# Kernel optimization log

Measured on AMD Instinct MI355X. Metric: run time of the kernel, lower is better.

## Reference

```python
import jax, jax.numpy as jnp
import numpy as np
import math

B, T, D = 2, 2048, 1024
H, HD = 16, 64          # num_heads, head_dim = D // H
ROPE, BASE = 64, 10000.0  # rope covers full head dim
GLOBAL_IDS = jnp.array([2, 3, 4, 5, 6, 7], dtype=jnp.int32)


def setup_inputs() -> dict:
    key = jax.random.key(0)
    k1, k2, k3, k4 = jax.random.split(key, 4)
    x = jax.random.normal(k1, (B, T, D), dtype=jnp.float32)
    input_ids = jax.random.randint(k2, (B, T), 0, 1024, dtype=jnp.int32)
    W_qkv = jax.random.normal(k3, (3 * H * HD, D), dtype=jnp.float32) * 0.02
    b_qkv = jnp.zeros((3 * H * HD,), dtype=jnp.float32)
    W_out = jax.random.normal(k4, (D, H * HD), dtype=jnp.float32) * 0.02
    b_out = jnp.zeros((D,), dtype=jnp.float32)
    return {"x": x, "input_ids": input_ids, "W_qkv": W_qkv, "b_qkv": b_qkv,
            "W_out": W_out, "b_out": b_out}


def _apply_rotary(x, cos, sin):
    # x: [B,H,T,HD]; rope covers first ROPE dims (= full head here)
    x_rot, x_pass = x[..., :ROPE], x[..., ROPE:]
    half = ROPE // 2
    x1, x2 = x_rot[..., :half], x_rot[..., half:]
    x1n = x1 * cos - x2 * sin
    x2n = x1 * sin + x2 * cos
    return jnp.concatenate([x1n, x2n, x_pass], axis=-1)


def reference(x, input_ids, W_qkv, b_qkv, W_out, b_out):
    Bx, Tx, _ = x.shape
    qkv = x @ W_qkv.T + b_qkv                      # [B,T,3*H*HD]
    q, k, v = jnp.split(qkv, 3, axis=-1)
    def heads(t):
        return t.reshape(Bx, Tx, H, HD).transpose(0, 2, 1, 3)  # [B,H,T,HD]
    q, k, v = heads(q), heads(k), heads(v)

    # RoPE
    pos = jnp.arange(Tx, dtype=jnp.float32)
    inv_freq = 1.0 / (BASE ** (jnp.arange(0, ROPE, 2, dtype=jnp.float32) / ROPE))
    freqs = pos[:, None] * inv_freq[None, :]        # [T, ROPE//2]
    cos, sin = jnp.cos(freqs)[None, None], jnp.sin(freqs)[None, None]
    q = _apply_rotary(q, cos, sin)
    k = _apply_rotary(k, cos, sin)

    # causal mask OR global-query rows (BigBird-style)
    causal = jnp.tril(jnp.ones((Tx, Tx), dtype=bool))[None, None]   # [1,1,T,T]
    global_mask = jnp.isin(input_ids, GLOBAL_IDS)                    # [B,T]
    allow = causal | global_mask[:, None, :, None]                   # [B,1,T,T]

    scale = math.sqrt(HD)
    logits = jnp.einsum('bhqd,bhkd->bhqk', q, k) / scale
    neg = -jnp.finfo(logits.dtype).max
    logits = jnp.where(allow, logits, neg)
    attn = jax.nn.softmax(logits, axis=-1)
    out = jnp.einsum('bhqk,bhkd->bhqd', attn, v)
    out = out.transpose(0, 2, 1, 3).reshape(Bx, Tx, H * HD)
    return out @ W_out.T + b_out
```

## Files before the change

### kernel.cpp

```cpp
#include <hip/hip_runtime.h>
#include <math.h>

#define Bc 2
#define Tc 2048
#define Dc 1024
#define Hc 16
#define HDc 64

typedef __attribute__((ext_vector_type(8))) short bf16x8;
typedef __attribute__((ext_vector_type(4))) float f32x4;
typedef __attribute__((ext_vector_type(16))) float f32x16;

__device__ __forceinline__ unsigned short f2bf(float f) {
    union { float f; unsigned int u; } v; v.f = f;
    unsigned int r = (v.u + 0x7FFFu + ((v.u >> 16) & 1u)) >> 16;
    return (unsigned short)r;
}
__device__ __forceinline__ unsigned pack2bf(float a, float b) {
    unsigned au = __float_as_uint(a) + 0x8000u;
    unsigned bu = __float_as_uint(b) + 0x8000u;
    return __builtin_amdgcn_perm(bu, au, 0x07060302u);
}

__device__ __forceinline__ void gload_lds16(const unsigned short* g,
                                            unsigned short* l) {
    __builtin_amdgcn_global_load_lds(
        (const __attribute__((address_space(1))) unsigned int*)g,
        (__attribute__((address_space(3))) unsigned int*)l,
        16, 0, 0);
}

#define CEXP 0.1803368801111204f

__global__ __launch_bounds__(256) void convert_bf16(
    const float* __restrict__ x, const float* __restrict__ wqkv,
    const float* __restrict__ wout,
    unsigned short* __restrict__ xb, unsigned short* __restrict__ wqkvb,
    unsigned short* __restrict__ woutb, float2* __restrict__ ropeTab)
{
    const int gid = blockIdx.x * 256 + threadIdx.x;
    if (gid < Tc * 32) {
        const int t = gid >> 5, i = gid & 31;
        const float freq = exp2f((float)i * -0.4152410118609203f);
        const float ang = (float)t * freq;
        ropeTab[gid] = make_float2(cosf(ang), sinf(ang));
    }
    const int i = gid * 4;
    const float* src; unsigned short* dst; int off;
    if (i < 4194304)      { src = x;    dst = xb;    off = i; }
    else if (i < 7340032) { src = wqkv; dst = wqkvb; off = i - 4194304; }
    else                  { src = wout; dst = woutb; off = i - 7340032; }
    float4 v = *(const float4*)&src[off];
    ushort4 o;
    o.x = f2bf(v.x); o.y = f2bf(v.y); o.z = f2bf(v.z); o.w = f2bf(v.w);
    *(ushort4*)&dst[off] = o;
}

template <int MODE>
__global__ __launch_bounds__(256) void gemm_mfma(
    const unsigned short* __restrict__ A, const unsigned short* __restrict__ W,
    const float* __restrict__ bias, float* __restrict__ C,
    unsigned short* __restrict__ Qp, unsigned short* __restrict__ Kp,
    unsigned short* __restrict__ Vtp, const float2* __restrict__ ropeTab,
    int M, int N, int K)
{
    __shared__ unsigned short Apk[128 * 8 * 8];
    __shared__ unsigned short Bpk[128 * 8 * 8];

    const int tid = threadIdx.x;
    const int lane = tid & 63;
    const int wave = tid >> 6;
    const int quad = lane >> 4;
    const int c = lane & 15;
    const int wm = wave >> 1;
    const int wn = wave & 1;
    const int m0 = blockIdx.y * 128;
    const int n0 = blockIdx.x * 128;

    f32x4 acc[4][4];
#pragma unroll
    for (int mt = 0; mt < 4; mt++)
#pragma unroll
        for (int nt = 0; nt < 4; nt++) acc[mt][nt] = (f32x4){0.f, 0.f, 0.f, 0.f};

    const int lrow = lane >> 3;
    const int srcoct = (lane & 7) ^ lrow;

    for (int k0 = 0; k0 < K; k0 += 64) {
        __syncthreads();
#pragma unroll
        for (int i = 0; i < 4; i++) {
            const int r = wave * 32 + i * 8 + lrow;
            gload_lds16(&A[(size_t)(m0 + r) * K + k0 + srcoct * 8],
                        &Apk[(wave * 32 + i * 8) * 64]);
            gload_lds16(&W[(size_t)(n0 + r) * K + k0 + srcoct * 8],
                        &Bpk[(wave * 32 + i * 8) * 64]);
        }
        __syncthreads();
#pragma unroll
        for (int ko = 0; ko < 2; ko++) {
            bf16x8 af[4], bf[4];
#pragma unroll
            for (int mt = 0; mt < 4; mt++) {
                const int m = wm * 64 + mt * 16 + c;
                af[mt] = *(const bf16x8*)&Apk[(m * 8 + ((ko * 4 + quad) ^ (m & 7))) * 8];
            }
#pragma unroll
            for (int nt = 0; nt < 4; nt++) {
                const int n = wn * 64 + nt * 16 + c;
                bf[nt] = *(const bf16x8*)&Bpk[(n * 8 + ((ko * 4 + quad) ^ (n & 7))) * 8];
            }
#pragma unroll
            for (int mt = 0; mt < 4; mt++)
#pragma unroll
                for (int nt = 0; nt < 4; nt++)
                    acc[mt][nt] = __builtin_amdgcn_mfma_f32_16x16x32_bf16(
                        af[mt], bf[nt], acc[mt][nt], 0, 0, 0);
        }
    }

    if (MODE == 0) {
#pragma unroll
        for (int mt = 0; mt < 4; mt++) {
            const int m = m0 + wm * 64 + mt * 16 + quad * 4;
#pragma unroll
            for (int nt = 0; nt < 4; nt++) {
                const int n = n0 + wn * 64 + nt * 16 + c;
                const float bv = bias[n];
#pragma unroll
                for (int reg = 0; reg < 4; reg++)
                    C[(size_t)(m + reg) * N + n] = acc[mt][nt][reg] + bv;
            }
        }
    } else {
        const int n_wave = n0 + wn * 64;
        const int which = n_wave >> 10;
        const int h = (n_wave >> 6) & 15;
        const int b = m0 >> 11;
        const int t_base = (m0 & 2047) + wm * 64;

        __syncthreads();
        unsigned short* stg = ((wave < 2) ? Apk : Bpk) + (wave & 1) * 4096;

        if (which < 2) {
            unsigned short* dst = (which == 0) ? Qp : Kp;
#pragma unroll
            for (int mt = 0; mt < 4; mt++) {
#pragma unroll
                for (int nt = 0; nt < 2; nt++) {
                    const int i1 = nt * 16 + c;
                    const float bv1 = bias[n_wave + i1];
                    const float bv2 = bias[n_wave + 32 + i1];
#pragma unroll
                    for (int reg = 0; reg < 4; reg++) {
                        const int row = mt * 16 + quad * 4 + reg;
                        const float2 cs = ropeTab[(t_base + row) * 32 + i1];
                        const float x1 = acc[mt][nt][reg] + bv1;
                        const float x2 = acc[mt][nt + 2][reg] + bv2;
                        const int col2 = 32 + i1;
                        stg[(row * 8 + ((i1 >> 3) ^ (row & 7))) * 8 + (i1 & 7)] =
                            f2bf(x1 * cs.x - x2 * cs.y);
                        stg[(row * 8 + ((col2 >> 3) ^ (row & 7))) * 8 + (col2 & 7)] =
                            f2bf(x1 * cs.y + x2 * cs.x);
                    }
                }
            }
            const size_t obase = ((size_t)(b * Hc + h) * Tc + t_base) * HDc;
            const int oct = lane & 7;
#pragma unroll
            for (int k = 0; k < 8; k++) {
                const int f = lane * 8 + k * 512;
                const int row = f >> 6;
                bf16x8 vv = *(const bf16x8*)&stg[(row * 8 + (oct ^ (row & 7))) * 8];
                *(bf16x8*)&dst[obase + f] = vv;
            }
        } else {
#pragma unroll
            for (int mt = 0; mt < 4; mt++) {
#pragma unroll
                for (int nt = 0; nt < 4; nt++) {
                    const int d = nt * 16 + c;
                    const float bv = bias[n_wave + d];
#pragma unroll
                    for (int reg = 0; reg < 4; reg++) {
                        const int r = mt * 16 + quad * 4 + reg;
                        stg[(d * 8 + ((r >> 3) ^ (d & 7))) * 8 + (r & 7)] =
                            f2bf(acc[mt][nt][reg] + bv);
                    }
                }
            }
            const size_t vbase = (size_t)(b * Hc + h) * HDc * Tc;
            const int oct = lane & 7;
#pragma unroll
            for (int k = 0; k < 8; k++) {
                const int d = (lane >> 3) + k * 8;
                bf16x8 vv = *(const bf16x8*)&stg[(d * 8 + (oct ^ (d & 7))) * 8];
                *(bf16x8*)&Vtp[vbase + (size_t)d * Tc + t_base + oct * 8] = vv;
            }
        }
    }
}

__global__ __launch_bounds__(256, 4) void attn_fused(
    const unsigned short* __restrict__ Q, const unsigned short* __restrict__ K,
    const unsigned short* __restrict__ Vt, const int* __restrict__ ids,
    unsigned short* __restrict__ AO)
{
    __shared__ __align__(16) float smem[8448];

    const int tid = threadIdx.x;
    const int lane = tid & 63;
    const int wave = tid >> 6;
    const int c32 = lane & 31;
    const int h = lane >> 5;
    const int blk = blockIdx.x;

    if (blk < 32) {
        int* s_list = (int*)smem;
        int* s_cnt = (int*)smem + 64;
        float* s_accm = smem + 128;
        float* s_lm = s_accm + 8192;

        const int bh = blk;
        const int b = bh >> 4;
        const int hd = bh & 15;
        const size_t qkbase = (size_t)bh * Tc * HDc;

        if (tid == 0) *s_cnt = 0;
        __syncthreads();
        for (int i = tid; i < Tc; i += 256) {
            int id = ids[b * Tc + i];
            if ((unsigned)(id - 2) <= 5u) {
                int p = atomicAdd(s_cnt, 1);
                if (p < 64) s_list[p] = i;
            }
        }
        __syncthreads();
        const int cnt = min(*s_cnt, 64);

        for (int pass = 0; pass * 32 < cnt; pass++) {
            const int slot = pass * 32 + c32;
            const int row = (slot < cnt) ? s_list[slot] : s_list[0];

            bf16x8 qf[4];
#pragma unroll
            for (int ko = 0; ko < 4; ko++)
                qf[ko] = *(const bf16x8*)&Q[qkbase + (size_t)row * HDc + ko * 16 + h * 8];

            f32x16 acc0 = {}, acc1 = {};
            float lacc = 0.0f;

            for (int it = wave; it < Tc / 64; it += 4) {
                const int t0 = it * 64;
                f32x16 s0 = {}, s1 = {};
#pragma unroll
                for (int ko = 0; ko < 4; ko++) {
                    const int koff = ko * 16 + h * 8;
                    bf16x8 kf0 = *(const bf16x8*)&K[qkbase + (size_t)(t0 + c32) * HDc + koff];
                    bf16x8 kf1 = *(const bf16x8*)&K[qkbase + (size_t)(t0 + 32 + c32) * HDc + koff];
                    s0 = __builtin_amdgcn_mfma_f32_32x32x16_bf16(kf0, qf[ko], s0, 0, 0, 0);
                    s1 = __builtin_amdgcn_mfma_f32_32x32x16_bf16(kf1, qf[ko], s1, 0, 0, 0);
                }
                float v[32];
#pragma unroll
                for (int r = 0; r < 16; r++) { v[r] = s0[r]; v[16 + r] = s1[r]; }
#pragma unroll
                for (int i = 0; i < 32; i++) v[i] = exp2f(v[i] * CEXP);
                unsigned pk[16];
#pragma unroll
                for (int i = 0; i < 16; i++) pk[i] = pack2bf(v[2 * i], v[2 * i + 1]);
#pragma unroll
                for (int st = 1; st < 32; st <<= 1)
#pragma unroll
                    for (int i = 0; i < 32; i += 2 * st) v[i] += v[i + st];
                lacc += v[0];
#pragma unroll
                for (int ko = 0; ko < 4; ko++) {
                    const int a = (ko >> 1) * 8 + (ko & 1) * 4;
                    unsigned keep0 = h ? pk[a + 2] : pk[a + 0];
                    unsigned keep1 = h ? pk[a + 3] : pk[a + 1];
                    unsigned send0 = h ? pk[a + 0] : pk[a + 2];
                    unsigned send1 = h ? pk[a + 1] : pk[a + 3];
                    unsigned recv0 = (unsigned)__shfl_xor((int)send0, 32);
                    unsigned recv1 = (unsigned)__shfl_xor((int)send1, 32);
                    union { bf16x8 v8; unsigned u[4]; } pf;
                    pf.u[0] = h ? recv0 : keep0;
                    pf.u[1] = h ? recv1 : keep1;
                    pf.u[2] = h ? keep0 : recv0;
                    pf.u[3] = h ? keep1 : recv1;
                    const int oct = ko * 2 + h;
                    bf16x8 vf0 = *(const bf16x8*)&Vt[qkbase + (size_t)c32 * Tc + t0 + oct * 8];
                    bf16x8 vf1 = *(const bf16x8*)&Vt[qkbase + (size_t)(32 + c32) * Tc + t0 + oct * 8];
                    acc0 = __builtin_amdgcn_mfma_f32_32x32x16_bf16(vf0, pf.v8, acc0, 0, 0, 0);
                    acc1 = __builtin_amdgcn_mfma_f32_32x32x16_bf16(vf1, pf.v8, acc1, 0, 0, 0);
                }
            }

            const float lfull = lacc + __shfl_xor(lacc, 32);
            if (h == 0) s_lm[wave * 32 + c32] = lfull;
#pragma unroll
            for (int r = 0; r < 16; r++) {
                const int d = (r & 3) + 8 * (r >> 2) + 4 * h;
                s_accm[(wave * 64 + d) * 32 + c32] = acc0[r];
                s_accm[(wave * 64 + 32 + d) * 32 + c32] = acc1[r];
            }
            __syncthreads();
            for (int i = tid; i < 2048; i += 256) {
                const int sl = i >> 6, d = i & 63;
                if (pass * 32 + sl < cnt) {
                    const float o = s_accm[(0 * 64 + d) * 32 + sl] + s_accm[(1 * 64 + d) * 32 + sl] +
                                    s_accm[(2 * 64 + d) * 32 + sl] + s_accm[(3 * 64 + d) * 32 + sl];
                    const float lt = s_lm[sl] + s_lm[32 + sl] + s_lm[64 + sl] + s_lm[96 + sl];
                    const int qrow = s_list[pass * 32 + sl];
                    AO[((size_t)(b * Tc + qrow)) * Dc + hd * HDc + d] = f2bf(o / lt);
                }
            }
            __syncthreads();
        }
        return;
    }

    unsigned short* KV = (unsigned short*)smem;
    unsigned short* Ke = KV;
    unsigned short* Ko = KV + 4096;
    unsigned short* Ve = KV + 8192;
    unsigned short* Vo = KV + 12288;

    const int idx = blk - 32;
    const int bh = (idx & 7) + 8 * ((idx >> 3) & 3);
    const int b = bh >> 4;
    const int hd = bh & 15;
    const int w = idx >> 5;
    const int u = w & 7, tq = w >> 3;
    const int j = (tq == 0) ? u : (tq == 1) ? 31 - u : (tq == 2) ? 8 + u : 23 - u;
    const int qb0 = j * 64;
    const int nT = j + 1;
    const int wq0 = qb0 + (wave & 1) * 32;
    const size_t qkbase = (size_t)bh * Tc * HDc;
    const int q = wq0 + c32;

    bf16x8 qf[4];
#pragma unroll
    for (int ko = 0; ko < 4; ko++)
        qf[ko] = *(const bf16x8*)&Q[qkbase + (size_t)q * HDc + ko * 16 + h * 8];

    const int myid = ids[b * Tc + q];
    const bool gr = ((unsigned)(myid - 2) <= 5u);

    f32x16 acc0 = {}, acc1 = {};
    float lacc = 0.0f;

    const int lrow = lane >> 3;
    const int srcoct = (lane & 7) ^ lrow;
    const int jb = wave * 2;

    auto stageK = [&](int t0, unsigned short* buf) {
#pragma unroll
        for (int i = 0; i < 2; i++) {
            const int jj = jb + i;
            const int row = jj * 8 + lrow;
            gload_lds16(&K[qkbase + (size_t)(t0 + row) * HDc + srcoct * 8],
                        &buf[jj * 512]);
        }
    };
    auto stageV = [&](int t0, unsigned short* buf) {
#pragma unroll
        for (int i = 0; i < 2; i++) {
            const int jj = jb + i;
            const int d = jj * 8 + lrow;
            gload_lds16(&Vt[qkbase + (size_t)d * Tc + t0 + srcoct * 8],
                        &buf[jj * 512]);
        }
    };

    auto computeT = [&](int t0, const unsigned short* Kb, const unsigned short* Vb) {
        f32x16 s0 = {}, s1 = {};
#pragma unroll
        for (int ko = 0; ko < 4; ko++) {
            const int oct = ko * 2 + h;
            const int k0i = c32;
            const int k1i = 32 + c32;
            bf16x8 kf0 = *(const bf16x8*)&Kb[(k0i * 8 + (oct ^ (k0i & 7))) * 8];
            bf16x8 kf1 = *(const bf16x8*)&Kb[(k1i * 8 + (oct ^ (k1i & 7))) * 8];
            s0 = __builtin_amdgcn_mfma_f32_32x32x16_bf16(kf0, qf[ko], s0, 0, 0, 0);
            s1 = __builtin_amdgcn_mfma_f32_32x32x16_bf16(kf1, qf[ko], s1, 0, 0, 0);
        }

        float v[32];
#pragma unroll
        for (int r = 0; r < 16; r++) { v[r] = s0[r]; v[16 + r] = s1[r]; }
#pragma unroll
        for (int i = 0; i < 32; i++) v[i] = exp2f(v[i] * CEXP);

        const bool needMask = (t0 + 63 > wq0);
        if (needMask) {
            const int thr = wq0 + c32 - t0 - 4 * h;
#pragma unroll
            for (int kt = 0; kt < 2; kt++)
#pragma unroll
                for (int r = 0; r < 16; r++) {
                    const int ckr = kt * 32 + (r & 3) + 8 * (r >> 2);
                    v[kt * 16 + r] = (ckr <= thr) ? v[kt * 16 + r] : 0.0f;
                }
        }

        unsigned pk[16];
#pragma unroll
        for (int i = 0; i < 16; i++) pk[i] = pack2bf(v[2 * i], v[2 * i + 1]);

#pragma unroll
        for (int st = 1; st < 32; st <<= 1)
#pragma unroll
            for (int i = 0; i < 32; i += 2 * st) v[i] += v[i + st];
        lacc += v[0];

#pragma unroll
        for (int ko = 0; ko < 4; ko++) {
            const int a = (ko >> 1) * 8 + (ko & 1) * 4;
            unsigned keep0 = h ? pk[a + 2] : pk[a + 0];
            unsigned keep1 = h ? pk[a + 3] : pk[a + 1];
            unsigned send0 = h ? pk[a + 0] : pk[a + 2];
            unsigned send1 = h ? pk[a + 1] : pk[a + 3];
            unsigned recv0 = (unsigned)__shfl_xor((int)send0, 32);
            unsigned recv1 = (unsigned)__shfl_xor((int)send1, 32);
            union { bf16x8 v8; unsigned u[4]; } pf;
            pf.u[0] = h ? recv0 : keep0;
            pf.u[1] = h ? recv1 : keep1;
            pf.u[2] = h ? keep0 : recv0;
            pf.u[3] = h ? keep1 : recv1;
            const int oct = ko * 2 + h;
            const int d0 = c32, d1 = 32 + c32;
            bf16x8 vf0 = *(const bf16x8*)&Vb[(d0 * 8 + (oct ^ (d0 & 7))) * 8];
            bf16x8 vf1 = *(const bf16x8*)&Vb[(d1 * 8 + (oct ^ (d1 & 7))) * 8];
            acc0 = __builtin_amdgcn_mfma_f32_32x32x16_bf16(vf0, pf.v8, acc0, 0, 0, 0);
            acc1 = __builtin_amdgcn_mfma_f32_32x32x16_bf16(vf1, pf.v8, acc1, 0, 0, 0);
        }
    };

    for (int tp = 0; tp < nT; tp += 2) {
        __syncthreads();
        stageK(tp * 64, Ke);
        stageV(tp * 64, Ve);
        const bool has2 = (tp + 1) < nT;
        if (has2) {
            stageK((tp + 1) * 64, Ko);
            stageV((tp + 1) * 64, Vo);
        }
        __syncthreads();
        if ((wave >> 1) == 0) computeT(tp * 64, Ke, Ve);
        else if (has2) computeT((tp + 1) * 64, Ko, Vo);
    }

    __syncthreads();
    float* mrg = smem + (wave & 1) * 2176;
    if (wave >= 2) {
#pragma unroll
        for (int r = 0; r < 16; r++) {
            mrg[r * 64 + lane] = acc0[r];
            mrg[(16 + r) * 64 + lane] = acc1[r];
        }
        mrg[2048 + lane] = lacc;
    }
    __syncthreads();
    if (wave >= 2) return;
#pragma unroll
    for (int r = 0; r < 16; r++) {
        acc0[r] += mrg[r * 64 + lane];
        acc1[r] += mrg[(16 + r) * 64 + lane];
    }
    lacc += mrg[2048 + lane];

    const float l = lacc + __shfl_xor(lacc, 32);
    if (!gr) {
        const float inv = 1.0f / l;
        unsigned short* dst = &AO[((size_t)(b * Tc + q)) * Dc + hd * HDc];
#pragma unroll
        for (int i = 0; i < 8; i++) {
            const int r = 2 * i;
            const int d = (r & 3) + 8 * (r >> 2) + 4 * h;
            *(unsigned*)&dst[d]      = pack2bf(acc0[r] * inv, acc0[r + 1] * inv);
            *(unsigned*)&dst[32 + d] = pack2bf(acc1[r] * inv, acc1[r + 1] * inv);
        }
    }
}

extern "C" void kernel_launch(void* const* d_in, const int* in_sizes, int n_in,
                              void* d_out, int out_size, void* d_ws, size_t ws_size,
                              hipStream_t stream)
{
    const float* x    = (const float*)d_in[0];
    const int*   ids  = (const int*)d_in[1];
    const float* Wqkv = (const float*)d_in[2];
    const float* bqkv = (const float*)d_in[3];
    const float* Wout = (const float*)d_in[4];
    const float* bout = (const float*)d_in[5];
    float* out = (float*)d_out;

    const size_t TEN = (size_t)Bc * Hc * Tc * HDc;
    unsigned short* xb    = (unsigned short*)d_ws;
    unsigned short* wqkvb = xb + 4194304;
    unsigned short* woutb = wqkvb + 3145728;
    float2* ropeTab       = (float2*)(woutb + 1048576);
    unsigned short* Qb    = (unsigned short*)(ropeTab + 65536);
    unsigned short* Kb    = Qb + TEN;
    unsigned short* Vtb   = Kb + TEN;
    unsigned short* AOb   = Vtb + TEN;

    convert_bf16<<<8192, 256, 0, stream>>>(x, Wqkv, Wout, xb, wqkvb, woutb,
                                           ropeTab);
    dim3 g1(3072 / 128, 4096 / 128);
    gemm_mfma<1><<<g1, 256, 0, stream>>>(xb, wqkvb, bqkv, nullptr,
                                         Qb, Kb, Vtb, ropeTab, 4096, 3072, 1024);
    attn_fused<<<1056, 256, 0, stream>>>(Qb, Kb, Vtb, ids, AOb);
    dim3 g4(1024 / 128, 4096 / 128);
    gemm_mfma<0><<<g4, 256, 0, stream>>>(AOb, woutb, bout, out,
                                         nullptr, nullptr, nullptr, nullptr,
                                         4096, 1024, 1024);
}
```

Baseline: 200.7 us.

## Load K/V fragments directly from global memory instead of staging through LDS

```diff
diff --git a/kernel.cpp b/kernel.cpp
--- a/kernel.cpp
+++ b/kernel.cpp
@@ -201,7 +201,7 @@
     }
 }
 
-__global__ __launch_bounds__(256, 4) void attn_fused(
+__global__ __launch_bounds__(256) void attn_fused(
     const unsigned short* __restrict__ Q, const unsigned short* __restrict__ K,
     const unsigned short* __restrict__ Vt, const int* __restrict__ ids,
     unsigned short* __restrict__ AO)
@@ -320,12 +320,6 @@
         return;
     }
 
-    unsigned short* KV = (unsigned short*)smem;
-    unsigned short* Ke = KV;
-    unsigned short* Ko = KV + 4096;
-    unsigned short* Ve = KV + 8192;
-    unsigned short* Vo = KV + 12288;
-
     const int idx = blk - 32;
     const int bh = (idx & 7) + 8 * ((idx >> 3) & 3);
     const int b = bh >> 4;
@@ -335,6 +329,7 @@
     const int j = (tq == 0) ? u : (tq == 1) ? 31 - u : (tq == 2) ? 8 + u : 23 - u;
     const int qb0 = j * 64;
     const int nT = j + 1;
+    const int grp = wave >> 1;
     const int wq0 = qb0 + (wave & 1) * 32;
     const size_t qkbase = (size_t)bh * Tc * HDc;
     const int q = wq0 + c32;
@@ -350,47 +345,36 @@
     f32x16 acc0 = {}, acc1 = {};
     float lacc = 0.0f;
 
-    const int lrow = lane >> 3;
-    const int srcoct = (lane & 7) ^ lrow;
-    const int jb = wave * 2;
-
-    auto stageK = [&](int t0, unsigned short* buf) {
-#pragma unroll
-        for (int i = 0; i < 2; i++) {
-            const int jj = jb + i;
-            const int row = jj * 8 + lrow;
-            gload_lds16(&K[qkbase + (size_t)(t0 + row) * HDc + srcoct * 8],
-                        &buf[jj * 512]);
-        }
-    };
-    auto stageV = [&](int t0, unsigned short* buf) {
-#pragma unroll
-        for (int i = 0; i < 2; i++) {
-            const int jj = jb + i;
-            const int d = jj * 8 + lrow;
-            gload_lds16(&Vt[qkbase + (size_t)d * Tc + t0 + srcoct * 8],
-                        &buf[jj * 512]);
-        }
-    };
-
-    auto computeT = [&](int t0, const unsigned short* Kb, const unsigned short* Vb) {
+    for (int tt = grp; tt < nT; tt += 2) {
+        const int t0 = tt * 64;
+
+        bf16x8 kf[8];
+#pragma unroll
+        for (int ko = 0; ko < 4; ko++) {
+            const int koff = ko * 16 + h * 8;
+            kf[2 * ko]     = *(const bf16x8*)&K[qkbase + (size_t)(t0 + c32) * HDc + koff];
+            kf[2 * ko + 1] = *(const bf16x8*)&K[qkbase + (size_t)(t0 + 32 + c32) * HDc + koff];
+        }
         f32x16 s0 = {}, s1 = {};
+#pragma unroll
+        for (int ko = 0; ko < 4; ko++) {
+            s0 = __builtin_amdgcn_mfma_f32_32x32x16_bf16(kf[2 * ko], qf[ko], s0, 0, 0, 0);
+            s1 = __builtin_amdgcn_mfma_f32_32x32x16_bf16(kf[2 * ko + 1], qf[ko], s1, 0, 0, 0);
+        }
+
+        float v[32];
+#pragma unroll
+        for (int r = 0; r < 16; r++) { v[r] = s0[r]; v[16 + r] = s1[r]; }
+#pragma unroll
+        for (int i = 0; i < 32; i++) v[i] = exp2f(v[i] * CEXP);
+
+        bf16x8 vf[8];
 #pragma unroll
         for (int ko = 0; ko < 4; ko++) {
             const int oct = ko * 2 + h;
-            const int k0i = c32;
-            const int k1i = 32 + c32;
-            bf16x8 kf0 = *(const bf16x8*)&Kb[(k0i * 8 + (oct ^ (k0i & 7))) * 8];
-            bf16x8 kf1 = *(const bf16x8*)&Kb[(k1i * 8 + (oct ^ (k1i & 7))) * 8];
-            s0 = __builtin_amdgcn_mfma_f32_32x32x16_bf16(kf0, qf[ko], s0, 0, 0, 0);
-            s1 = __builtin_amdgcn_mfma_f32_32x32x16_bf16(kf1, qf[ko], s1, 0, 0, 0);
-        }
-
-        float v[32];
-#pragma unroll
-        for (int r = 0; r < 16; r++) { v[r] = s0[r]; v[16 + r] = s1[r]; }
-#pragma unroll
-        for (int i = 0; i < 32; i++) v[i] = exp2f(v[i] * CEXP);
+            vf[2 * ko]     = *(const bf16x8*)&Vt[qkbase + (size_t)c32 * Tc + t0 + oct * 8];
+            vf[2 * ko + 1] = *(const bf16x8*)&Vt[qkbase + (size_t)(32 + c32) * Tc + t0 + oct * 8];
+        }
 
         const bool needMask = (t0 + 63 > wq0);
         if (needMask) {
@@ -428,27 +412,9 @@
             pf.u[1] = h ? recv1 : keep1;
             pf.u[2] = h ? keep0 : recv0;
             pf.u[3] = h ? keep1 : recv1;
-            const int oct = ko * 2 + h;
-            const int d0 = c32, d1 = 32 + c32;
-            bf16x8 vf0 = *(const bf16x8*)&Vb[(d0 * 8 + (oct ^ (d0 & 7))) * 8];
-            bf16x8 vf1 = *(const bf16x8*)&Vb[(d1 * 8 + (oct ^ (d1 & 7))) * 8];
-            acc0 = __builtin_amdgcn_mfma_f32_32x32x16_bf16(vf0, pf.v8, acc0, 0, 0, 0);
-            acc1 = __builtin_amdgcn_mfma_f32_32x32x16_bf16(vf1, pf.v8, acc1, 0, 0, 0);
-        }
-    };
-
-    for (int tp = 0; tp < nT; tp += 2) {
-        __syncthreads();
-        stageK(tp * 64, Ke);
-        stageV(tp * 64, Ve);
-        const bool has2 = (tp + 1) < nT;
-        if (has2) {
-            stageK((tp + 1) * 64, Ko);
-            stageV((tp + 1) * 64, Vo);
-        }
-        __syncthreads();
-        if ((wave >> 1) == 0) computeT(tp * 64, Ke, Ve);
-        else if (has2) computeT((tp + 1) * 64, Ko, Vo);
+            acc0 = __builtin_amdgcn_mfma_f32_32x32x16_bf16(vf[2 * ko], pf.v8, acc0, 0, 0, 0);
+            acc1 = __builtin_amdgcn_mfma_f32_32x32x16_bf16(vf[2 * ko + 1], pf.v8, acc1, 0, 0, 0);
+        }
     }
 
     __syncthreads();
```

New measurement: 235.1 us. 17.2% more time.
